# Optimization experiments

Measured on AMD Instinct MI355X. Metric: run time of the kernel, lower is better.

## Reference

```python
import jax, jax.numpy as jnp
import numpy as np

B, I, O, T, L = 16, 512, 512, 256, 4096
EPS = 1e-8


def setup_inputs() -> dict:
    key = jax.random.key(0)
    ks = jax.random.split(key, 10)
    def lin_w(k, out_d, in_d):  # kaiming-uniform-ish init like torch Linear
        bound = 1.0 / np.sqrt(in_d)
        return jax.random.uniform(k, (out_d, in_d), jnp.float32, -bound, bound)
    return {
        "x": jax.random.normal(ks[0], (B, I, L), jnp.float32),
        "t": jax.random.normal(ks[1], (B, T), jnp.float32),
        "weight": lin_w(ks[2], O, I),            # base conv weight [O, I]
        "W1": lin_w(ks[3], T, T), "b1": jnp.zeros((T,), jnp.float32),
        "W2": lin_w(ks[4], T, T), "b2": jnp.zeros((T,), jnp.float32),
        "W3": lin_w(ks[5], I, T), "b3": jnp.zeros((I,), jnp.float32),
    }


def reference(x, t, weight, W1, b1, W2, b2, W3, b3):
    # mod MLP: Linear -> SiLU -> Linear -> SiLU -> Linear
    h = jax.nn.silu(t @ W1.T + b1)
    h = jax.nn.silu(h @ W2.T + b2)
    s = h @ W3.T + b3 + 1.0                    # [B, I] modulation scales
    bw = weight[None, :, :] * s[:, None, :]    # [B, O, I]
    demod = jax.lax.rsqrt(jnp.sum(bw * bw, axis=2) + EPS)  # [B, O]
    bw = bw * demod[:, :, None]                # demodulated per-sample weights
    # grouped 1x1 conv (groups=B) == batched pointwise contraction
    return jnp.einsum('boi,bil->bol', bw, x)   # [B, O, L]
```

## Files before the change

### kernel.cpp

```cpp
#include <hip/hip_runtime.h>
#include <hip/hip_bf16.h>

typedef float f4v __attribute__((ext_vector_type(4)));
typedef float f32x4 __attribute__((ext_vector_type(4)));
typedef __bf16 bf16x8 __attribute__((ext_vector_type(8)));

#define GLDS16(gsrc, ldst)                                                  \
  __builtin_amdgcn_global_load_lds(                                         \
      (const __attribute__((address_space(1))) unsigned int*)(gsrc),        \
      (__attribute__((address_space(3))) unsigned int*)(ldst), 16, 0, 0)

__device__ __forceinline__ unsigned pack2bf(float lo, float hi) {
  unsigned short ua = __builtin_bit_cast(unsigned short, (__bf16)lo);
  unsigned short ub = __builtin_bit_cast(unsigned short, (__bf16)hi);
  return (unsigned)ua | ((unsigned)ub << 16);
}

__global__ __launch_bounds__(256) void mlp_kernel(
    const float* __restrict__ t,
    const float* __restrict__ W1, const float* __restrict__ b1,
    const float* __restrict__ W2, const float* __restrict__ b2,
    const float* __restrict__ W3, const float* __restrict__ b3,
    float* __restrict__ s_out) {
  __shared__ float tt[256];
  __shared__ float hh[256];
  const int b = blockIdx.x;
  const int tid = threadIdx.x;
  tt[tid] = t[b * 256 + tid];
  __syncthreads();
  float acc = b1[tid];
  {
    const f4v* wrow = (const f4v*)(W1 + tid * 256);
    #pragma unroll 16
    for (int k = 0; k < 64; ++k) {
      f4v wv = wrow[k];
      acc += wv[0] * tt[4 * k] + wv[1] * tt[4 * k + 1] +
             wv[2] * tt[4 * k + 2] + wv[3] * tt[4 * k + 3];
    }
  }
  float h = acc / (1.0f + expf(-acc));
  __syncthreads();
  hh[tid] = h;
  __syncthreads();
  acc = b2[tid];
  {
    const f4v* wrow = (const f4v*)(W2 + tid * 256);
    #pragma unroll 16
    for (int k = 0; k < 64; ++k) {
      f4v wv = wrow[k];
      acc += wv[0] * hh[4 * k] + wv[1] * hh[4 * k + 1] +
             wv[2] * hh[4 * k + 2] + wv[3] * hh[4 * k + 3];
    }
  }
  h = acc / (1.0f + expf(-acc));
  __syncthreads();
  tt[tid] = h;
  __syncthreads();
  #pragma unroll
  for (int rep = 0; rep < 2; ++rep) {
    const int o = rep * 256 + tid;
    float a3 = b3[o];
    const f4v* wrow = (const f4v*)(W3 + o * 256);
    #pragma unroll 16
    for (int k = 0; k < 64; ++k) {
      f4v wv = wrow[k];
      a3 += wv[0] * tt[4 * k] + wv[1] * tt[4 * k + 1] +
            wv[2] * tt[4 * k + 2] + wv[3] * tt[4 * k + 3];
    }
    s_out[b * 512 + o] = a3 + 1.0f;
  }
}

__global__ __launch_bounds__(256) void modw_kernel(
    const float* __restrict__ weight, const float* __restrict__ s_in,
    unsigned short* __restrict__ bwq) {
  const int tid = threadIdx.x;
  const int wid = (blockIdx.x << 2) | (tid >> 6);
  const int b = wid >> 9;
  const int o = wid & 511;
  const int lane = tid & 63;
  const f4v* wp = (const f4v*)(weight + o * 512 + lane * 8);
  const f4v* sp = (const f4v*)(s_in + b * 512 + lane * 8);
  f4v w0 = wp[0], w1 = wp[1];
  f4v s0 = sp[0], s1 = sp[1];
  float p[8];
  p[0] = w0[0] * s0[0]; p[1] = w0[1] * s0[1];
  p[2] = w0[2] * s0[2]; p[3] = w0[3] * s0[3];
  p[4] = w1[0] * s1[0]; p[5] = w1[1] * s1[1];
  p[6] = w1[2] * s1[2]; p[7] = w1[3] * s1[3];
  float ss = 0.0f;
  #pragma unroll
  for (int i = 0; i < 8; ++i) ss += p[i] * p[i];
  #pragma unroll
  for (int off = 32; off; off >>= 1) ss += __shfl_xor(ss, off);
  const float d = rsqrtf(ss + 1e-8f);
  uint4 outw;
  outw.x = pack2bf(p[0] * d, p[1] * d);
  outw.y = pack2bf(p[2] * d, p[3] * d);
  outw.z = pack2bf(p[4] * d, p[5] * d);
  outw.w = pack2bf(p[6] * d, p[7] * d);
  *(uint4*)(bwq + ((size_t)(b * 512 + o)) * 512 + lane * 8) = outw;
}

__global__ __launch_bounds__(256) void gemm_kernel(
    const float* __restrict__ x, const unsigned short* __restrict__ bwq,
    float* __restrict__ out) {
  __shared__ __align__(16) unsigned short As[2][4096];
  __shared__ __align__(16) float Bs[2][4096];

  const int bid = blockIdx.x;
  const int swz = ((bid & 7) << 8) | (bid >> 3);
  const int mt = swz & 3;
  const int nt = (swz >> 2) & 31;
  const int bb = swz >> 7;

  const int tid = threadIdx.x;
  const int lane = tid & 63;
  const int wv = tid >> 6;
  const int wr = wv >> 1, wc = wv & 1;

  const unsigned short* abase = bwq + ((size_t)(bb * 512 + mt * 128)) * 512;
  const float* xbase = x + ((size_t)bb * 512) * 4096 + nt * 128;

  const int s0 = tid, s1 = 256 + tid;
  const int kq0 = s0 >> 7, p0 = s0 & 127;
  const int kq1 = s1 >> 7, p1 = s1 & 127;
  const int i0 = p0 ^ ((p0 >> 3) & 7);
  const int i1 = p1 ^ ((p1 >> 3) & 7);
  const unsigned short* asrc0 = abase + i0 * 512 + kq0 * 8;
  const unsigned short* asrc1 = abase + i1 * 512 + kq1 * 8;

  const float* bsrc[4];
  #pragma unroll
  for (int r = 0; r < 4; ++r) {
    const int sl = tid + 256 * r;
    const int k = sl >> 5;
    const int gp = sl & 31;
    const int gl = gp ^ (((k >> 3) & 1) << 2);
    bsrc[r] = xbase + (size_t)k * 4096 + gl * 4;
  }

  const int kqL = lane >> 4;
  const int rL = lane & 15;
  int aro[4];
  #pragma unroll
  for (int i = 0; i < 4; ++i) {
    const int m = wr * 64 + i * 16 + rL;
    aro[i] = kqL * 2048 + (m ^ ((m >> 3) & 7)) * 16;
  }
  int bro[4];
  #pragma unroll
  for (int i = 0; i < 4; ++i) {
    const int nb = wc * 64 + i * 16 + rL;
    const int g = (nb >> 2) ^ ((kqL & 1) << 2);
    bro[i] = kqL * 1024 + g * 4 + (nb & 3);
  }

  f32x4 acc[4][4] = {};

#define STAGE(IT, BUF)                                                      \
  do {                                                                      \
    const int _ko = (IT) * 32;                                              \
    GLDS16(asrc0 + _ko, &As[BUF][s0 * 8]);                                  \
    GLDS16(asrc1 + _ko, &As[BUF][s1 * 8]);                                  \
    GLDS16(bsrc[0] + (size_t)_ko * 4096, &Bs[BUF][(tid + 0) * 4]);          \
    GLDS16(bsrc[1] + (size_t)_ko * 4096, &Bs[BUF][(tid + 256) * 4]);        \
    GLDS16(bsrc[2] + (size_t)_ko * 4096, &Bs[BUF][(tid + 512) * 4]);        \
    GLDS16(bsrc[3] + (size_t)_ko * 4096, &Bs[BUF][(tid + 768) * 4]);        \
  } while (0)

  STAGE(0, 0);
  __syncthreads();

  #pragma unroll
  for (int it = 0; it < 16; ++it) {
    const int cur = it & 1;
    if (it < 15) STAGE(it + 1, cur ^ 1);

    {
      const char* ab = (const char*)&As[cur][0];
      const float* bbuf = &Bs[cur][0];
      bf16x8 a0 = *(const bf16x8*)(ab + aro[0]);
      bf16x8 a1 = *(const bf16x8*)(ab + aro[1]);
      bf16x8 a2 = *(const bf16x8*)(ab + aro[2]);
      bf16x8 a3 = *(const bf16x8*)(ab + aro[3]);
      #pragma unroll
      for (int ni = 0; ni < 4; ++ni) {
        const float* bp = bbuf + bro[ni];
        bf16x8 bf;
        bf[0] = (__bf16)bp[0 * 128];
        bf[1] = (__bf16)bp[1 * 128];
        bf[2] = (__bf16)bp[2 * 128];
        bf[3] = (__bf16)bp[3 * 128];
        bf[4] = (__bf16)bp[4 * 128];
        bf[5] = (__bf16)bp[5 * 128];
        bf[6] = (__bf16)bp[6 * 128];
        bf[7] = (__bf16)bp[7 * 128];
        acc[0][ni] = __builtin_amdgcn_mfma_f32_16x16x32_bf16(a0, bf, acc[0][ni], 0, 0, 0);
        acc[1][ni] = __builtin_amdgcn_mfma_f32_16x16x32_bf16(a1, bf, acc[1][ni], 0, 0, 0);
        acc[2][ni] = __builtin_amdgcn_mfma_f32_16x16x32_bf16(a2, bf, acc[2][ni], 0, 0, 0);
        acc[3][ni] = __builtin_amdgcn_mfma_f32_16x16x32_bf16(a3, bf, acc[3][ni], 0, 0, 0);
      }
    }
    __syncthreads();
  }

  const size_t ob =
      ((size_t)(bb * 512 + mt * 128 + wr * 64 + ((lane >> 4) << 2))) * 4096 +
      nt * 128 + wc * 64 + (lane & 15);
  #pragma unroll
  for (int mi = 0; mi < 4; ++mi)
    #pragma unroll
    for (int ni = 0; ni < 4; ++ni)
      #pragma unroll
      for (int jj = 0; jj < 4; ++jj)
        out[ob + (size_t)(mi * 16 + jj) * 4096 + ni * 16] = acc[mi][ni][jj];

#undef STAGE
}

extern "C" void kernel_launch(void* const* d_in, const int* in_sizes, int n_in,
                              void* d_out, int out_size, void* d_ws, size_t ws_size,
                              hipStream_t stream) {
  const float* x      = (const float*)d_in[0];
  const float* t      = (const float*)d_in[1];
  const float* weight = (const float*)d_in[2];
  const float* W1     = (const float*)d_in[3];
  const float* b1     = (const float*)d_in[4];
  const float* W2     = (const float*)d_in[5];
  const float* b2     = (const float*)d_in[6];
  const float* W3     = (const float*)d_in[7];
  const float* b3     = (const float*)d_in[8];
  float* out = (float*)d_out;

  float* s_ws = (float*)d_ws;
  unsigned short* bwq = (unsigned short*)((char*)d_ws + 32 * 1024);

  mlp_kernel<<<16, 256, 0, stream>>>(t, W1, b1, W2, b2, W3, b3, s_ws);
  modw_kernel<<<2048, 256, 0, stream>>>(weight, s_ws, bwq);
  gemm_kernel<<<2048, 256, 0, stream>>>(x, bwq, out);
}
```

Baseline: 144.3 us.

## Load GEMM operands to registers and pack x to bf16 in per-wave LDS

Replaces the async global-to-LDS staging of fp32 x and bf16 weights with direct register loads. The A fragments are read straight from global memory, and x is converted to bf16 once and written into a per-wave swizzled LDS region. Because each wave owns its own LDS slice, the block-wide barriers go away, LDS traffic and footprint shrink, and launch bounds now request two blocks per SIMD. In exchange the kernel holds more registers (two stages of x and A in flight) and issues redundant A loads across waves, with no block-level sharing of the weight tile.

Measured after the change: 171.4 us. 18.7% more time.

```diff
diff --git a/kernel.cpp b/kernel.cpp
--- a/kernel.cpp
+++ b/kernel.cpp
@@ -4,11 +4,6 @@
 typedef float f4v __attribute__((ext_vector_type(4)));
 typedef float f32x4 __attribute__((ext_vector_type(4)));
 typedef __bf16 bf16x8 __attribute__((ext_vector_type(8)));
-
-#define GLDS16(gsrc, ldst)                                                  \
-  __builtin_amdgcn_global_load_lds(                                         \
-      (const __attribute__((address_space(1))) unsigned int*)(gsrc),        \
-      (__attribute__((address_space(3))) unsigned int*)(ldst), 16, 0, 0)
 
 __device__ __forceinline__ unsigned pack2bf(float lo, float hi) {
   unsigned short ua = __builtin_bit_cast(unsigned short, (__bf16)lo);
@@ -102,11 +97,10 @@
   *(uint4*)(bwq + ((size_t)(b * 512 + o)) * 512 + lane * 8) = outw;
 }
 
-__global__ __launch_bounds__(256) void gemm_kernel(
+__global__ __launch_bounds__(256, 2) void gemm_kernel(
     const float* __restrict__ x, const unsigned short* __restrict__ bwq,
     float* __restrict__ out) {
-  __shared__ __align__(16) unsigned short As[2][4096];
-  __shared__ __align__(16) float Bs[2][4096];
+  __shared__ __align__(16) unsigned short BsArr[2][4][2048];
 
   const int bid = blockIdx.x;
   const int swz = ((bid & 7) << 8) | (bid >> 3);
@@ -119,91 +113,100 @@
   const int wv = tid >> 6;
   const int wr = wv >> 1, wc = wv & 1;
 
-  const unsigned short* abase = bwq + ((size_t)(bb * 512 + mt * 128)) * 512;
-  const float* xbase = x + ((size_t)bb * 512) * 4096 + nt * 128;
-
-  const int s0 = tid, s1 = 256 + tid;
-  const int kq0 = s0 >> 7, p0 = s0 & 127;
-  const int kq1 = s1 >> 7, p1 = s1 & 127;
-  const int i0 = p0 ^ ((p0 >> 3) & 7);
-  const int i1 = p1 ^ ((p1 >> 3) & 7);
-  const unsigned short* asrc0 = abase + i0 * 512 + kq0 * 8;
-  const unsigned short* asrc1 = abase + i1 * 512 + kq1 * 8;
-
-  const float* bsrc[4];
-  #pragma unroll
-  for (int r = 0; r < 4; ++r) {
-    const int sl = tid + 256 * r;
-    const int k = sl >> 5;
-    const int gp = sl & 31;
-    const int gl = gp ^ (((k >> 3) & 1) << 2);
-    bsrc[r] = xbase + (size_t)k * 4096 + gl * 4;
-  }
-
+  const int rL = lane & 15;
   const int kqL = lane >> 4;
-  const int rL = lane & 15;
-  int aro[4];
-  #pragma unroll
-  for (int i = 0; i < 4; ++i) {
-    const int m = wr * 64 + i * 16 + rL;
-    aro[i] = kqL * 2048 + (m ^ ((m >> 3) & 7)) * 16;
-  }
+  const int q = lane & 15;
+  const int kb = lane >> 4;
+
+  const float* xlane = x + ((size_t)bb * 512 + kb * 8) * 4096 +
+                       nt * 128 + wc * 64 + q * 4;
+  const unsigned short* abase =
+      bwq + ((size_t)(bb * 512 + mt * 128 + wr * 64)) * 512;
+  const unsigned short* aptr[4];
+  #pragma unroll
+  for (int mi = 0; mi < 4; ++mi)
+    aptr[mi] = abase + (mi * 16 + rL) * 512 + kqL * 8;
+
   int bro[4];
   #pragma unroll
-  for (int i = 0; i < 4; ++i) {
-    const int nb = wc * 64 + i * 16 + rL;
-    const int g = (nb >> 2) ^ ((kqL & 1) << 2);
-    bro[i] = kqL * 1024 + g * 4 + (nb & 3);
-  }
+  for (int ni = 0; ni < 4; ++ni)
+    bro[ni] = (ni * 16 + rL) * 32 + ((kqL * 8) ^ ((rL & 3) * 8));
 
   f32x4 acc[4][4] = {};
-
-#define STAGE(IT, BUF)                                                      \
-  do {                                                                      \
-    const int _ko = (IT) * 32;                                              \
-    GLDS16(asrc0 + _ko, &As[BUF][s0 * 8]);                                  \
-    GLDS16(asrc1 + _ko, &As[BUF][s1 * 8]);                                  \
-    GLDS16(bsrc[0] + (size_t)_ko * 4096, &Bs[BUF][(tid + 0) * 4]);          \
-    GLDS16(bsrc[1] + (size_t)_ko * 4096, &Bs[BUF][(tid + 256) * 4]);        \
-    GLDS16(bsrc[2] + (size_t)_ko * 4096, &Bs[BUF][(tid + 512) * 4]);        \
-    GLDS16(bsrc[3] + (size_t)_ko * 4096, &Bs[BUF][(tid + 768) * 4]);        \
-  } while (0)
-
-  STAGE(0, 0);
-  __syncthreads();
-
-  #pragma unroll
-  for (int it = 0; it < 16; ++it) {
-    const int cur = it & 1;
-    if (it < 15) STAGE(it + 1, cur ^ 1);
-
-    {
-      const char* ab = (const char*)&As[cur][0];
-      const float* bbuf = &Bs[cur][0];
-      bf16x8 a0 = *(const bf16x8*)(ab + aro[0]);
-      bf16x8 a1 = *(const bf16x8*)(ab + aro[1]);
-      bf16x8 a2 = *(const bf16x8*)(ab + aro[2]);
-      bf16x8 a3 = *(const bf16x8*)(ab + aro[3]);
-      #pragma unroll
-      for (int ni = 0; ni < 4; ++ni) {
-        const float* bp = bbuf + bro[ni];
-        bf16x8 bf;
-        bf[0] = (__bf16)bp[0 * 128];
-        bf[1] = (__bf16)bp[1 * 128];
-        bf[2] = (__bf16)bp[2 * 128];
-        bf[3] = (__bf16)bp[3 * 128];
-        bf[4] = (__bf16)bp[4 * 128];
-        bf[5] = (__bf16)bp[5 * 128];
-        bf[6] = (__bf16)bp[6 * 128];
-        bf[7] = (__bf16)bp[7 * 128];
-        acc[0][ni] = __builtin_amdgcn_mfma_f32_16x16x32_bf16(a0, bf, acc[0][ni], 0, 0, 0);
-        acc[1][ni] = __builtin_amdgcn_mfma_f32_16x16x32_bf16(a1, bf, acc[1][ni], 0, 0, 0);
-        acc[2][ni] = __builtin_amdgcn_mfma_f32_16x16x32_bf16(a2, bf, acc[2][ni], 0, 0, 0);
-        acc[3][ni] = __builtin_amdgcn_mfma_f32_16x16x32_bf16(a3, bf, acc[3][ni], 0, 0, 0);
-      }
-    }
-    __syncthreads();
-  }
+  f4v xv[2][8];
+  bf16x8 fv[2][4];
+
+#define XLOAD(P, IT)                                                        \
+  do {                                                                      \
+    _Pragma("unroll")                                                       \
+    for (int j = 0; j < 8; ++j)                                             \
+      xv[P][j] = *(const f4v*)(xlane + ((size_t)((IT) * 32) + j) * 4096);   \
+  } while (0)
+
+#define ALOAD(P, IT)                                                        \
+  do {                                                                      \
+    _Pragma("unroll")                                                       \
+    for (int mi = 0; mi < 4; ++mi)                                          \
+      fv[P][mi] = *(const bf16x8*)(aptr[mi] + (IT) * 32);                   \
+  } while (0)
+
+#define PACK(P, BUF)                                                        \
+  do {                                                                      \
+    unsigned short* wbw = &BsArr[BUF][wv][0];                               \
+    _Pragma("unroll")                                                       \
+    for (int c = 0; c < 4; ++c) {                                           \
+      _Pragma("unroll")                                                     \
+      for (int h = 0; h < 2; ++h) {                                         \
+        uint2 val;                                                          \
+        val.x = pack2bf(xv[P][h * 4 + 0][c], xv[P][h * 4 + 1][c]);          \
+        val.y = pack2bf(xv[P][h * 4 + 2][c], xv[P][h * 4 + 3][c]);          \
+        *(uint2*)&wbw[(q * 4 + c) * 32 + ((kb * 8 + h * 4) ^ (c * 8))] = val; \
+      }                                                                     \
+    }                                                                       \
+  } while (0)
+
+#define COMPUTE(P, BUF)                                                     \
+  do {                                                                      \
+    const unsigned short* wb = &BsArr[BUF][wv][0];                          \
+    bf16x8 b0 = *(const bf16x8*)(wb + bro[0]);                              \
+    bf16x8 b1 = *(const bf16x8*)(wb + bro[1]);                              \
+    bf16x8 b2 = *(const bf16x8*)(wb + bro[2]);                              \
+    bf16x8 b3 = *(const bf16x8*)(wb + bro[3]);                              \
+    acc[0][0] = __builtin_amdgcn_mfma_f32_16x16x32_bf16(fv[P][0], b0, acc[0][0], 0, 0, 0); \
+    acc[0][1] = __builtin_amdgcn_mfma_f32_16x16x32_bf16(fv[P][0], b1, acc[0][1], 0, 0, 0); \
+    acc[0][2] = __builtin_amdgcn_mfma_f32_16x16x32_bf16(fv[P][0], b2, acc[0][2], 0, 0, 0); \
+    acc[0][3] = __builtin_amdgcn_mfma_f32_16x16x32_bf16(fv[P][0], b3, acc[0][3], 0, 0, 0); \
+    acc[1][0] = __builtin_amdgcn_mfma_f32_16x16x32_bf16(fv[P][1], b0, acc[1][0], 0, 0, 0); \
+    acc[1][1] = __builtin_amdgcn_mfma_f32_16x16x32_bf16(fv[P][1], b1, acc[1][1], 0, 0, 0); \
+    acc[1][2] = __builtin_amdgcn_mfma_f32_16x16x32_bf16(fv[P][1], b2, acc[1][2], 0, 0, 0); \
+    acc[1][3] = __builtin_amdgcn_mfma_f32_16x16x32_bf16(fv[P][1], b3, acc[1][3], 0, 0, 0); \
+    acc[2][0] = __builtin_amdgcn_mfma_f32_16x16x32_bf16(fv[P][2], b0, acc[2][0], 0, 0, 0); \
+    acc[2][1] = __builtin_amdgcn_mfma_f32_16x16x32_bf16(fv[P][2], b1, acc[2][1], 0, 0, 0); \
+    acc[2][2] = __builtin_amdgcn_mfma_f32_16x16x32_bf16(fv[P][2], b2, acc[2][2], 0, 0, 0); \
+    acc[2][3] = __builtin_amdgcn_mfma_f32_16x16x32_bf16(fv[P][2], b3, acc[2][3], 0, 0, 0); \
+    acc[3][0] = __builtin_amdgcn_mfma_f32_16x16x32_bf16(fv[P][3], b0, acc[3][0], 0, 0, 0); \
+    acc[3][1] = __builtin_amdgcn_mfma_f32_16x16x32_bf16(fv[P][3], b1, acc[3][1], 0, 0, 0); \
+    acc[3][2] = __builtin_amdgcn_mfma_f32_16x16x32_bf16(fv[P][3], b2, acc[3][2], 0, 0, 0); \
+    acc[3][3] = __builtin_amdgcn_mfma_f32_16x16x32_bf16(fv[P][3], b3, acc[3][3], 0, 0, 0); \
+  } while (0)
+
+#define STEP(IT, P, Q)                                                      \
+  do {                                                                      \
+    if ((IT) + 1 < 16) ALOAD(Q, (IT) + 1);                                  \
+    if ((IT) + 2 < 16) XLOAD(P, (IT) + 2);                                  \
+    if ((IT) + 1 < 16) PACK(Q, ((IT) + 1) & 1);                             \
+    COMPUTE(P, (IT) & 1);                                                   \
+  } while (0)
+
+  XLOAD(0, 0);
+  XLOAD(1, 1);
+  ALOAD(0, 0);
+  PACK(0, 0);
+
+  STEP(0, 0, 1);  STEP(1, 1, 0);  STEP(2, 0, 1);  STEP(3, 1, 0);
+  STEP(4, 0, 1);  STEP(5, 1, 0);  STEP(6, 0, 1);  STEP(7, 1, 0);
+  STEP(8, 0, 1);  STEP(9, 1, 0);  STEP(10, 0, 1); STEP(11, 1, 0);
+  STEP(12, 0, 1); STEP(13, 1, 0); STEP(14, 0, 1); STEP(15, 1, 0);
 
   const size_t ob =
       ((size_t)(bb * 512 + mt * 128 + wr * 64 + ((lane >> 4) << 2))) * 4096 +
@@ -216,7 +219,11 @@
       for (int jj = 0; jj < 4; ++jj)
         out[ob + (size_t)(mi * 16 + jj) * 4096 + ni * 16] = acc[mi][ni][jj];
 
-#undef STAGE
+#undef XLOAD
+#undef ALOAD
+#undef PACK
+#undef COMPUTE
+#undef STEP
 }
 
 extern "C" void kernel_launch(void* const* d_in, const int* in_sizes, int n_in,
```
